# Performance work log

Hardware: AMD Instinct MI355X
Metric: run time of the kernel (lower is better)

The kernel has to match this reference:

```python
import jax, jax.numpy as jnp
import numpy as np

NUM_HEADS = 8
D_MODEL = 256
DIM = D_MODEL // NUM_HEADS  # 32
EPS = 1e-6


def _proj(x, W, b):
    # Conv1d with kernel_size=1 == channel-mixing matmul over length axis
    return jnp.einsum('oi,bil->bol', W, x) + b[None, :, None]


def _linear_attention(q, k, v):
    # q,k,v: [B, dim, heads, L]
    q = jax.nn.elu(q) + 1.0
    k = jax.nn.elu(k) + 1.0
    L = v.shape[3]
    v = v / L
    # KV: [B, dim_v, dim_k, heads]
    KV = jnp.einsum('bdhm,bqhm->bqdh', k, v)
    # Z: [B, heads, L]
    Z = 1.0 / (jnp.einsum('bdhm,bdh->bhm', q, k.sum(3)) + EPS)
    # out: [B, dim, heads, L]
    return jnp.einsum('bdhm,bqdh,bhm->bqhm', q, KV, Z) * L


def setup_inputs() -> dict:
    key = jax.random.key(0)
    ks = jax.random.split(key, 11)
    B, L = 8, 4096
    s = 0.05
    return {
        'query': jax.random.normal(ks[0], (B, D_MODEL, L), dtype=jnp.float32),
        'key':   jax.random.normal(ks[1], (B, D_MODEL, L), dtype=jnp.float32),
        'value': jax.random.normal(ks[2], (B, D_MODEL, L), dtype=jnp.float32),
        'Wq': jax.random.normal(ks[3], (D_MODEL, D_MODEL), dtype=jnp.float32) * s,
        'bq': jnp.zeros((D_MODEL,), dtype=jnp.float32),
        'Wk': jax.random.normal(ks[4], (D_MODEL, D_MODEL), dtype=jnp.float32) * s,
        'bk': jnp.zeros((D_MODEL,), dtype=jnp.float32),
        'Wv': jax.random.normal(ks[5], (D_MODEL, D_MODEL), dtype=jnp.float32) * s,
        'bv': jnp.zeros((D_MODEL,), dtype=jnp.float32),
        'Wm': jax.random.normal(ks[6], (D_MODEL, D_MODEL), dtype=jnp.float32) * s,
        'bm': jnp.zeros((D_MODEL,), dtype=jnp.float32),
    }


def reference(query, key, value, Wq, bq, Wk, bk, Wv, bv, Wm, bm):
    B = query.shape[0]
    q = _proj(query, Wq, bq).reshape(B, DIM, NUM_HEADS, -1)
    k = _proj(key,   Wk, bk).reshape(B, DIM, NUM_HEADS, -1)
    v = _proj(value, Wv, bv).reshape(B, DIM, NUM_HEADS, -1)
    x = _linear_attention(q, k, v)           # [B, dim, heads, L]
    x = x.reshape(B, D_MODEL, -1)            # merge heads back to channels
    return jnp.einsum('oi,bil->bol', Wm, x) + bm[None, :, None]
```

## Files before the change

kernel.cpp:

```cpp
#include <hip/hip_runtime.h>
#include <math.h>

#define D_MODEL 256
#define NHEADS 8
#define HDIM 32
#define BATCH 8
#define SEQL 4096
#define EPS 1e-6f

typedef _Float16 f16;
typedef _Float16 f16x4 __attribute__((ext_vector_type(4)));
typedef _Float16 f16x8 __attribute__((ext_vector_type(8)));
typedef float f32x4 __attribute__((ext_vector_type(4)));

__device__ __forceinline__ float elu1(float x) {
    return x > 0.f ? x + 1.f : __expf(x);
}

__global__ void prep_kernel(const float* __restrict__ Wq, const float* __restrict__ Wk,
                            const float* __restrict__ Wv, const float* __restrict__ Wm,
                            const float* __restrict__ bq, const float* __restrict__ bk,
                            const float* __restrict__ bv,
                            f16* __restrict__ w16, float* __restrict__ bperm) {
    const int bid = blockIdx.x;
    if (bid < 1024) {
        int idx = bid * 256 + threadIdx.x;
        int mat = idx >> 16;
        int r = idx & 65535;
        int e = r & 7;
        int lane = (r >> 3) & 63;
        int kstep = (r >> 9) & 7;
        int ostrip = r >> 12;
        int o = ostrip * 16 + (lane & 15);
        int k = kstep * 32 + (lane >> 4) * 8 + e;
        const float* W = (mat == 0) ? Wq : (mat == 1) ? Wk : (mat == 2) ? Wv : Wm;
        float v;
        if (mat < 3) v = W[(size_t)(((o & 31) << 3) + (o >> 5)) * 256 + k];
        else         v = W[(size_t)o * 256 + (((k & 31) << 3) + (k >> 5))];
        w16[idx] = (f16)v;
    } else {
        int t = threadIdx.x;
        bperm[0 * 256 + t] = bq[((t & 31) << 3) + (t >> 5)];
        bperm[1 * 256 + t] = bk[((t & 31) << 3) + (t >> 5)];
        bperm[2 * 256 + t] = bv[((t & 31) << 3) + (t >> 5)];
    }
}

#define XSTR 264
__global__ __launch_bounds__(256, 3) void gemm_stage1(
    const float* __restrict__ Xq, const float* __restrict__ Xk, const float* __restrict__ Xv,
    const f16* __restrict__ w16, const float* __restrict__ bperm,
    f16* __restrict__ yq, f16* __restrict__ yk, f16* __restrict__ yv) {
    __shared__ __align__(16) f16 Xs[64 * XSTR];
    f16* Cb = Xs;

    const int z = blockIdx.z;
    const int which = z >> 3;
    const int b = z & 7;
    const float* X = (which == 0) ? Xq : (which == 1) ? Xk : Xv;
    const f16* W = w16 + which * 65536;
    f16* Y = (which == 0) ? yq : (which == 1) ? yk : yv;
    const float* bp = bperm + which * 256;

    const int l0 = blockIdx.x * 64;
    const int tid = threadIdx.x;
    const int wave = tid >> 6, lane = tid & 63;
    const int ln = lane & 15, quad = lane >> 4;
    const int kq = tid & 15;
    const int lg = tid >> 4;

    const float* Xbase = X + ((size_t)(b * D_MODEL) + 4 * kq) * SEQL + l0 + 4 * lg;

    float4 xa[4], xb[4];

#define LOADX(DST, C) do { \
        const float* xp_ = Xbase + (size_t)(64 * (C)) * SEQL; \
        DST[0] = *(const float4*)(xp_ + 0 * SEQL); \
        DST[1] = *(const float4*)(xp_ + 1 * SEQL); \
        DST[2] = *(const float4*)(xp_ + 2 * SEQL); \
        DST[3] = *(const float4*)(xp_ + 3 * SEQL); \
    } while (0)

#define STOREB(SRC, C) do { \
        f16x4 w_; \
        w_[0] = (f16)SRC[0].x; w_[1] = (f16)SRC[1].x; w_[2] = (f16)SRC[2].x; w_[3] = (f16)SRC[3].x; \
        *(f16x4*)&Xs[(4 * lg + 0) * XSTR + 64 * (C) + 4 * kq] = w_; \
        w_[0] = (f16)SRC[0].y; w_[1] = (f16)SRC[1].y; w_[2] = (f16)SRC[2].y; w_[3] = (f16)SRC[3].y; \
        *(f16x4*)&Xs[(4 * lg + 1) * XSTR + 64 * (C) + 4 * kq] = w_; \
        w_[0] = (f16)SRC[0].z; w_[1] = (f16)SRC[1].z; w_[2] = (f16)SRC[2].z; w_[3] = (f16)SRC[3].z; \
        *(f16x4*)&Xs[(4 * lg + 2) * XSTR + 64 * (C) + 4 * kq] = w_; \
        w_[0] = (f16)SRC[0].w; w_[1] = (f16)SRC[1].w; w_[2] = (f16)SRC[2].w; w_[3] = (f16)SRC[3].w; \
        *(f16x4*)&Xs[(4 * lg + 3) * XSTR + 64 * (C) + 4 * kq] = w_; \
    } while (0)

    f32x4 acc[4][4];
#pragma unroll
    for (int mf = 0; mf < 4; ++mf)
#pragma unroll
        for (int nf = 0; nf < 4; ++nf)
#pragma unroll
            for (int r = 0; r < 4; ++r) acc[mf][nf][r] = 0.f;

    LOADX(xa, 0);
    LOADX(xb, 1);
    STOREB(xa, 0);
    LOADX(xa, 2);
    STOREB(xb, 1);
    LOADX(xb, 3);
    STOREB(xa, 2);
    STOREB(xb, 3);
    __syncthreads();

    const f16* Wl = W + lane * 8;
    f16x8 afc[4], afn[4];
#pragma unroll
    for (int mf = 0; mf < 4; ++mf)
        afc[mf] = *(const f16x8*)(Wl + (wave * 32 + mf * 8 + 0) * 512);
#pragma unroll
    for (int s = 0; s < 8; ++s) {
        const int k0 = s * 32;
        if (s < 7) {
#pragma unroll
            for (int mf = 0; mf < 4; ++mf)
                afn[mf] = *(const f16x8*)(Wl + (wave * 32 + mf * 8 + s + 1) * 512);
        }
        f16x8 bf[4];
#pragma unroll
        for (int nf = 0; nf < 4; ++nf)
            bf[nf] = *(const f16x8*)&Xs[(nf * 16 + ln) * XSTR + k0 + quad * 8];
#pragma unroll
        for (int mf = 0; mf < 4; ++mf)
#pragma unroll
            for (int nf = 0; nf < 4; ++nf)
                acc[mf][nf] = __builtin_amdgcn_mfma_f32_16x16x32_f16(afc[mf], bf[nf], acc[mf][nf], 0, 0, 0);
#pragma unroll
        for (int mf = 0; mf < 4; ++mf) afc[mf] = afn[mf];
    }

    float bv_[4][4];
#pragma unroll
    for (int mf = 0; mf < 4; ++mf)
#pragma unroll
        for (int r = 0; r < 4; ++r)
            bv_[mf][r] = bp[wave * 64 + mf * 16 + quad * 4 + r];
    __syncthreads();
#pragma unroll
    for (int mf = 0; mf < 4; ++mf)
#pragma unroll
        for (int nf = 0; nf < 4; ++nf) {
            f16x4 w;
#pragma unroll
            for (int r = 0; r < 4; ++r) w[r] = (f16)(acc[mf][nf][r] + bv_[mf][r]);
            *(f16x4*)&Cb[(nf * 16 + ln) * XSTR + wave * 64 + mf * 16 + quad * 4] = w;
        }
    __syncthreads();
    {
        const int l = tid >> 2, sg = tid & 3;
        f16* yr = Y + ((size_t)(b * SEQL + l0 + l)) * 256 + sg * 64;
#pragma unroll
        for (int u = 0; u < 8; ++u)
            *(f16x8*)(yr + u * 8) = *(const f16x8*)&Cb[l * XSTR + sg * 64 + u * 8];
    }
#undef LOADX
#undef STOREB
}

#define KVLP 66
__global__ __launch_bounds__(256) void kv_mfma(
    const f16* __restrict__ kp, const f16* __restrict__ vp,
    float* __restrict__ KVpart, float* __restrict__ ksum_part) {
    __shared__ __align__(16) f16 kT[32 * KVLP];
    __shared__ __align__(16) f16 vT[48 * KVLP];
    const int ls = blockIdx.x;
    const int bh = blockIdx.y;
    const int b = bh >> 3, h = bh & 7;
    const int t = threadIdx.x;
    const int wave = t >> 6, lane = t & 63;
    const int ln = lane & 15, quad = lane >> 4;
    const int lrow = t >> 2, seg = t & 3;

    {
        const int rr = 32 + (t >> 4), c0 = (t & 15) * 4;
        f16x4 w;
        const f16 one = (f16)1.f, zero = (f16)0.f;
        w[0] = w[1] = w[2] = w[3] = (rr == 32) ? one : zero;
        *(f16x4*)&vT[rr * KVLP + c0] = w;
    }

    const int tiP = wave >> 1, tjP = wave & 1;
    f32x4 accP, accS;
#pragma unroll
    for (int r = 0; r < 4; ++r) { accP[r] = 0.f; accS[r] = 0.f; }

    for (int ch = 0; ch < 8; ++ch) {
        __syncthreads();
        const size_t goff = ((size_t)(b * SEQL + ls * 512 + ch * 64 + lrow)) * 256 + h * 32 + seg * 8;
        f16x8 k8 = *(const f16x8*)(kp + goff);
        f16x8 v8 = *(const f16x8*)(vp + goff);
#pragma unroll
        for (int j = 0; j < 8; ++j) {
            kT[(seg * 8 + j) * KVLP + lrow] = (f16)elu1((float)k8[j]);
            vT[(seg * 8 + j) * KVLP + lrow] = v8[j];
        }
        __syncthreads();
#pragma unroll
        for (int ks = 0; ks < 2; ++ks) {
            const int kc = ks * 32 + quad * 8;
            f16x8 bP = *(const f16x8*)&kT[(tjP * 16 + ln) * KVLP + kc];
            f16x8 aP = *(const f16x8*)&vT[(tiP * 16 + ln) * KVLP + kc];
            accP = __builtin_amdgcn_mfma_f32_16x16x32_f16(aP, bP, accP, 0, 0, 0);
            if (wave < 2) {
                f16x8 aS = *(const f16x8*)&vT[(32 + ln) * KVLP + kc];
                accS = __builtin_amdgcn_mfma_f32_16x16x32_f16(aS, bP, accS, 0, 0, 0);
            }
        }
    }

    float* KVp = KVpart + ((size_t)ls * 64 + bh) * 1024;
#pragma unroll
    for (int r = 0; r < 4; ++r)
        KVp[(tiP * 16 + quad * 4 + r) * 32 + tjP * 16 + ln] = accP[r];
    if (wave < 2 && quad == 0)
        ksum_part[((size_t)ls * 64 + bh) * 32 + tjP * 16 + ln] = accS[0];
}

__global__ __launch_bounds__(256) void kv_reduce(
    const float* __restrict__ KVpart, const float* __restrict__ ksum_part,
    float* __restrict__ KVfin, float* __restrict__ ksum_f) {
    const int bh = blockIdx.x;
    const int t = threadIdx.x;
    const float* src = KVpart + (size_t)bh * 1024 + t * 4;
    float ax = 0.f, ay = 0.f, az = 0.f, aw = 0.f;
#pragma unroll
    for (int s = 0; s < 8; ++s) {
        float4 p = *(const float4*)(src + (size_t)s * 65536);
        ax += p.x; ay += p.y; az += p.z; aw += p.w;
    }
    float4 o; o.x = ax; o.y = ay; o.z = az; o.w = aw;
    *(float4*)(KVfin + (size_t)bh * 1024 + t * 4) = o;
    if (t < 32) {
        float ss = 0.f;
#pragma unroll
        for (int s = 0; s < 8; ++s)
            ss += ksum_part[((size_t)s * 64 + bh) * 32 + t];
        ksum_f[bh * 32 + t] = ss;
    }
}

__global__ __launch_bounds__(256) void attn_out_kernel(
    const f16* __restrict__ qp, const float* __restrict__ KV,
    const float* __restrict__ ksum, const f16* __restrict__ wm16,
    const float* __restrict__ bm, float* __restrict__ out) {
    __shared__ __align__(16) f16 xs[64 * 264];
    __shared__ __align__(16) f16 Baug[8 * 48 * 40];
    __shared__ float dens[8][64];
    const int b = blockIdx.y;
    const int l0 = blockIdx.x * 64;
    const int t = threadIdx.x;
    const int wave = t >> 6, lane = t & 63;
    const int ln = lane & 15, quad = lane >> 4;

    {
        const int h = t >> 5, qd = t & 31;
        const float* kvp = KV + ((size_t)(b * NHEADS + h) * HDIM + qd) * HDIM;
        f16* dst = &Baug[(h * 48 + qd) * 40];
#pragma unroll
        for (int i = 0; i < 32; i += 4) {
            float4 a = *(const float4*)(kvp + i);
            f16x4 w4;
            w4[0] = (f16)a.x; w4[1] = (f16)a.y; w4[2] = (f16)a.z; w4[3] = (f16)a.w;
            *(f16x4*)(dst + i) = w4;
        }
        Baug[(h * 48 + 32) * 40 + qd] = (f16)ksum[(size_t)(b * NHEADS + h) * HDIM + qd];
    }
    {
        const int rbase = t >> 5, ch = (t & 31) * 8;
        const f16* qr = qp + ((size_t)(b * SEQL + l0 + rbase)) * 256 + ch;
        f16* dst = &xs[rbase * 264 + ch];
#pragma unroll
        for (int p = 0; p < 8; ++p) {
            f16x8 v = *(const f16x8*)(qr + (size_t)(p * 8) * 256);
            f16x8 w;
#pragma unroll
            for (int j = 0; j < 8; ++j) w[j] = (f16)elu1((float)v[j]);
            *(f16x8*)(dst + p * 8 * 264) = w;
        }
    }
    __syncthreads();
#pragma unroll
    for (int hh = 0; hh < 2; ++hh) {
        const int h = wave * 2 + hh;
        f16x8 a_s[4], b_s[3];
#pragma unroll
        for (int mf = 0; mf < 4; ++mf)
            a_s[mf] = *(const f16x8*)&xs[(mf * 16 + ln) * 264 + h * 32 + quad * 8];
#pragma unroll
        for (int nf = 0; nf < 3; ++nf)
            b_s[nf] = *(const f16x8*)&Baug[(h * 48 + nf * 16 + ln) * 40 + quad * 8];
        f32x4 C[4][3];
#pragma unroll
        for (int mf = 0; mf < 4; ++mf)
#pragma unroll
            for (int nf = 0; nf < 3; ++nf) {
#pragma unroll
                for (int r = 0; r < 4; ++r) C[mf][nf][r] = 0.f;
                C[mf][nf] = __builtin_amdgcn_mfma_f32_16x16x32_f16(a_s[mf], b_s[nf], C[mf][nf], 0, 0, 0);
            }
        if (ln == 0) {
#pragma unroll
            for (int mf = 0; mf < 4; ++mf)
#pragma unroll
                for (int r = 0; r < 4; ++r)
                    dens[h][mf * 16 + quad * 4 + r] = C[mf][2][r];
        }
        __syncthreads();
#pragma unroll
        for (int mf = 0; mf < 4; ++mf)
#pragma unroll
            for (int r = 0; r < 4; ++r) {
                const int l = mf * 16 + quad * 4 + r;
                const float rd = __builtin_amdgcn_rcpf(dens[h][l] + EPS);
#pragma unroll
                for (int nf = 0; nf < 2; ++nf)
                    xs[l * 264 + h * 32 + nf * 16 + ln] = (f16)(C[mf][nf][r] * rd);
            }
        __syncthreads();
    }
    f32x4 acc[4][4];
#pragma unroll
    for (int mf = 0; mf < 4; ++mf)
#pragma unroll
        for (int nf = 0; nf < 4; ++nf)
#pragma unroll
            for (int r = 0; r < 4; ++r) acc[mf][nf][r] = 0.f;
    const f16* Wl = wm16 + lane * 8;
    f16x8 afc[4], afn[4];
#pragma unroll
    for (int mf = 0; mf < 4; ++mf)
        afc[mf] = *(const f16x8*)(Wl + (wave * 32 + mf * 8 + 0) * 512);
#pragma unroll
    for (int it = 0; it < 8; ++it) {
        const int k0 = it * 32;
        if (it < 7) {
#pragma unroll
            for (int mf = 0; mf < 4; ++mf)
                afn[mf] = *(const f16x8*)(Wl + (wave * 32 + mf * 8 + it + 1) * 512);
        }
        f16x8 bf[4];
#pragma unroll
        for (int nf = 0; nf < 4; ++nf)
            bf[nf] = *(const f16x8*)&xs[(nf * 16 + ln) * 264 + k0 + quad * 8];
#pragma unroll
        for (int mf = 0; mf < 4; ++mf)
#pragma unroll
            for (int nf = 0; nf < 4; ++nf)
                acc[mf][nf] = __builtin_amdgcn_mfma_f32_16x16x32_f16(afc[mf], bf[nf], acc[mf][nf], 0, 0, 0);
#pragma unroll
        for (int mf = 0; mf < 4; ++mf) afc[mf] = afn[mf];
    }
#pragma unroll
    for (int mf = 0; mf < 4; ++mf) {
        const int o = wave * 64 + mf * 16 + quad * 4;
#pragma unroll
        for (int r = 0; r < 4; ++r) {
            const float bb = bm[o + r];
            float* op = out + ((size_t)(b * D_MODEL + o + r)) * SEQL + l0;
#pragma unroll
            for (int nf = 0; nf < 4; ++nf)
                op[nf * 16 + ln] = acc[mf][nf][r] + bb;
        }
    }
}

extern "C" void kernel_launch(void* const* d_in, const int* in_sizes, int n_in,
                              void* d_out, int out_size, void* d_ws, size_t ws_size,
                              hipStream_t stream) {
    const float* query = (const float*)d_in[0];
    const float* key_  = (const float*)d_in[1];
    const float* value = (const float*)d_in[2];
    const float* Wq = (const float*)d_in[3];
    const float* bq = (const float*)d_in[4];
    const float* Wk = (const float*)d_in[5];
    const float* bk = (const float*)d_in[6];
    const float* Wv = (const float*)d_in[7];
    const float* bv = (const float*)d_in[8];
    const float* Wm = (const float*)d_in[9];
    const float* bm = (const float*)d_in[10];

    char* w = (char*)d_ws;
    f16*   w16    = (f16*)w;
    float* bperm  = (float*)(w + 524288);
    float* KVpart = (float*)(w + 528384);
    float* ksum_p = (float*)(w + 2625536);
    float* KVfin  = (float*)(w + 2691072);
    float* ksum_f = (float*)(w + 2953216);
    f16*   qp     = (f16*)(w + 2961408);
    f16*   kp     = qp + (size_t)BATCH * SEQL * 256;
    f16*   vp     = kp + (size_t)BATCH * SEQL * 256;

    prep_kernel<<<1025, 256, 0, stream>>>(Wq, Wk, Wv, Wm, bq, bk, bv, w16, bperm);

    gemm_stage1<<<dim3(SEQL / 64, 1, 24), 256, 0, stream>>>(
        query, key_, value, w16, bperm, qp, kp, vp);

    kv_mfma<<<dim3(8, BATCH * NHEADS), 256, 0, stream>>>(kp, vp, KVpart, ksum_p);

    kv_reduce<<<dim3(BATCH * NHEADS), 256, 0, stream>>>(KVpart, ksum_p, KVfin, ksum_f);

    attn_out_kernel<<<dim3(SEQL / 64, BATCH), 256, 0, stream>>>(
        qp, KVfin, ksum_f, w16 + 3 * 65536, bm, (float*)d_out);
}
```

Baseline: 199.4 us.

## Split KV reduction wider, stage output through LDS, raise stage1 occupancy hint

The KV accumulation kernel now splits the sequence into 16 chunks instead of 8, launching twice as many blocks so more CUs are busy, and the reduce kernel sums 16 partials. The output projection now stages results through shared memory in two halves and writes coalesced float4 rows instead of scattered scalar stores. The projection GEMM's launch bound is raised from 3 to 4 blocks per SIMD-group hint, which may force register spilling. Workspace offsets are shifted to fit the larger partial buffers.

After: 208.6 us. +4.6%, slower.

```diff
diff --git a/kernel.cpp b/kernel.cpp
--- a/kernel.cpp
+++ b/kernel.cpp
@@ -47,7 +47,7 @@
 }
 
 #define XSTR 264
-__global__ __launch_bounds__(256, 3) void gemm_stage1(
+__global__ __launch_bounds__(256, 4) void gemm_stage1(
     const float* __restrict__ Xq, const float* __restrict__ Xk, const float* __restrict__ Xv,
     const f16* __restrict__ w16, const float* __restrict__ bperm,
     f16* __restrict__ yq, f16* __restrict__ yk, f16* __restrict__ yv) {
@@ -166,6 +166,7 @@
 }
 
 #define KVLP 66
+#define NSPLIT 16
 __global__ __launch_bounds__(256) void kv_mfma(
     const f16* __restrict__ kp, const f16* __restrict__ vp,
     float* __restrict__ KVpart, float* __restrict__ ksum_part) {
@@ -192,9 +193,9 @@
 #pragma unroll
     for (int r = 0; r < 4; ++r) { accP[r] = 0.f; accS[r] = 0.f; }
 
-    for (int ch = 0; ch < 8; ++ch) {
-        __syncthreads();
-        const size_t goff = ((size_t)(b * SEQL + ls * 512 + ch * 64 + lrow)) * 256 + h * 32 + seg * 8;
+    for (int ch = 0; ch < 4; ++ch) {
+        __syncthreads();
+        const size_t goff = ((size_t)(b * SEQL + ls * 256 + ch * 64 + lrow)) * 256 + h * 32 + seg * 8;
         f16x8 k8 = *(const f16x8*)(kp + goff);
         f16x8 v8 = *(const f16x8*)(vp + goff);
 #pragma unroll
@@ -232,7 +233,7 @@
     const float* src = KVpart + (size_t)bh * 1024 + t * 4;
     float ax = 0.f, ay = 0.f, az = 0.f, aw = 0.f;
 #pragma unroll
-    for (int s = 0; s < 8; ++s) {
+    for (int s = 0; s < NSPLIT; ++s) {
         float4 p = *(const float4*)(src + (size_t)s * 65536);
         ax += p.x; ay += p.y; az += p.z; aw += p.w;
     }
@@ -241,7 +242,7 @@
     if (t < 32) {
         float ss = 0.f;
 #pragma unroll
-        for (int s = 0; s < 8; ++s)
+        for (int s = 0; s < NSPLIT; ++s)
             ss += ksum_part[((size_t)s * 64 + bh) * 32 + t];
         ksum_f[bh * 32 + t] = ss;
     }
@@ -358,17 +359,35 @@
 #pragma unroll
         for (int mf = 0; mf < 4; ++mf) afc[mf] = afn[mf];
     }
-#pragma unroll
-    for (int mf = 0; mf < 4; ++mf) {
-        const int o = wave * 64 + mf * 16 + quad * 4;
-#pragma unroll
-        for (int r = 0; r < 4; ++r) {
-            const float bb = bm[o + r];
-            float* op = out + ((size_t)(b * D_MODEL + o + r)) * SEQL + l0;
-#pragma unroll
-            for (int nf = 0; nf < 4; ++nf)
-                op[nf * 16 + ln] = acc[mf][nf][r] + bb;
-        }
+    float* Of = (float*)xs;
+    __syncthreads();
+#pragma unroll
+    for (int p = 0; p < 2; ++p) {
+        if ((wave >> 1) == p) {
+            const int rb = (wave & 1) * 64;
+#pragma unroll
+            for (int mf = 0; mf < 4; ++mf)
+#pragma unroll
+                for (int r = 0; r < 4; ++r) {
+                    const int o = wave * 64 + mf * 16 + quad * 4 + r;
+                    const float bb = bm[o];
+                    const int row = rb + mf * 16 + quad * 4 + r;
+#pragma unroll
+                    for (int nf = 0; nf < 4; ++nf)
+                        Of[row * 66 + nf * 16 + ln] = acc[mf][nf][r] + bb;
+                }
+        }
+        __syncthreads();
+        {
+            const int rw = t >> 4, lc = (t & 15) * 4;
+#pragma unroll
+            for (int rnd = 0; rnd < 8; ++rnd) {
+                const int row = rnd * 16 + rw;
+                float4 v4 = *(const float4*)&Of[row * 66 + lc];
+                *(float4*)(out + ((size_t)(b * D_MODEL + p * 128 + row)) * SEQL + l0 + lc) = v4;
+            }
+        }
+        __syncthreads();
     }
 }
 
@@ -391,10 +410,10 @@
     f16*   w16    = (f16*)w;
     float* bperm  = (float*)(w + 524288);
     float* KVpart = (float*)(w + 528384);
-    float* ksum_p = (float*)(w + 2625536);
-    float* KVfin  = (float*)(w + 2691072);
-    float* ksum_f = (float*)(w + 2953216);
-    f16*   qp     = (f16*)(w + 2961408);
+    float* ksum_p = (float*)(w + 4722688);
+    float* KVfin  = (float*)(w + 4853760);
+    float* ksum_f = (float*)(w + 5115904);
+    f16*   qp     = (f16*)(w + 5124096);
     f16*   kp     = qp + (size_t)BATCH * SEQL * 256;
     f16*   vp     = kp + (size_t)BATCH * SEQL * 256;
 
@@ -403,7 +422,7 @@
     gemm_stage1<<<dim3(SEQL / 64, 1, 24), 256, 0, stream>>>(
         query, key_, value, w16, bperm, qp, kp, vp);
 
-    kv_mfma<<<dim3(8, BATCH * NHEADS), 256, 0, stream>>>(kp, vp, KVpart, ksum_p);
+    kv_mfma<<<dim3(NSPLIT, BATCH * NHEADS), 256, 0, stream>>>(kp, vp, KVpart, ksum_p);
 
     kv_reduce<<<dim3(BATCH * NHEADS), 256, 0, stream>>>(KVpart, ksum_p, KVfin, ksum_f);
 
```
